# Performance work log

Hardware: AMD Instinct MI355X
Metric: run time of the kernel (lower is better)

Reference implementation:

```python
import jax, jax.numpy as jnp
import numpy as np

KV_LEN = 4096      # sliding-window length (init kv_len)
PAGE_SIZE = 16
SHIFT = 16         # hard-coded eviction shift in prefill_draft
BSZ = 4
SEQ_LEN = 512
HEADS = 16
HEAD_DIM = 128
PAGES = BSZ * KV_LEN // PAGE_SIZE  # 1024
ROPE_THETA = 10000.0


def _rope(x, positions):
    """Neox-style rotate-half RoPE. x: [B, L, H, D], positions: [L]."""
    d = x.shape[-1]
    inv_freq = 1.0 / (ROPE_THETA ** (jnp.arange(0, d, 2, dtype=jnp.float32) / d))  # [D/2]
    ang = positions.astype(jnp.float32)[:, None] * inv_freq[None, :]               # [L, D/2]
    cos = jnp.cos(ang)[None, :, None, :].astype(x.dtype)
    sin = jnp.sin(ang)[None, :, None, :].astype(x.dtype)
    x1, x2 = x[..., : d // 2], x[..., d // 2 :]
    return jnp.concatenate([x1 * cos - x2 * sin, x1 * sin + x2 * cos], axis=-1)


def setup_inputs() -> dict:
    key = jax.random.key(0)
    k1, k2, k3 = jax.random.split(key, 3)
    return {
        "k": jax.random.normal(k1, (BSZ * SEQ_LEN, HEADS, HEAD_DIM), jnp.float32),
        "v": jax.random.normal(k2, (BSZ * SEQ_LEN, HEADS, HEAD_DIM), jnp.float32),
        "draft_cache": jax.random.normal(k3, (PAGES, 2, PAGE_SIZE, HEADS, HEAD_DIM), jnp.float32),
        "kv_page_indices": jnp.arange(PAGES, dtype=jnp.int32),
        "bsz": BSZ,
        "context_len": KV_LEN,
        "seq_len": SEQ_LEN,
        "n_local_heads": HEADS,
        "head_dim": HEAD_DIM,
    }


def reference(k, v, draft_cache, kv_page_indices, bsz, context_len, seq_len, n_local_heads, head_dim):
    # Eviction branch of KVCache.prefill_draft (context_len + seq_len > kv_len):
    # gather paged cache -> sliding-window shift by SHIFT -> append new k/v -> re-RoPE keys -> scatter back to pages.
    pages_per_seq = kv_page_indices.shape[0] // bsz
    pages = kv_page_indices.reshape(bsz, pages_per_seq)                     # [B, P]
    # gather pages into per-sequence linear view: [B, 2, L, H, D]
    cache = draft_cache[pages]                                              # [B, P, 2, page, H, D]
    cache = jnp.transpose(cache, (0, 2, 1, 3, 4, 5)).reshape(
        bsz, 2, pages_per_seq * PAGE_SIZE, n_local_heads, head_dim)
    k_out, v_out = cache[:, 0], cache[:, 1]                                 # [B, L, H, D]

    k_val = k.reshape(bsz, seq_len, n_local_heads, head_dim)
    v_val = v.reshape(bsz, seq_len, n_local_heads, head_dim)

    keep = KV_LEN - SHIFT
    # shift window by SHIFT, append new tokens, keep last (kv_len - 16)
    new_k = jnp.concatenate([k_out[:, SHIFT:KV_LEN], k_val], axis=1)[:, -keep:]
    new_v = jnp.concatenate([v_out[:, SHIFT:KV_LEN], v_val], axis=1)[:, -keep:]

    k_full = k_out.at[:, :keep].set(new_k)
    v_full = v_out.at[:, :keep].set(new_v)

    # re-apply RoPE over the first kv_len key positions (offsets are zeros -> positions 0..kv_len-1)
    pos = jnp.arange(KV_LEN, dtype=jnp.int32)
    k_full = k_full.at[:, :KV_LEN].set(_rope(k_full[:, :KV_LEN], pos))

    # scatter back to paged layout: [max_num_pages, 2, page_size, H, D]
    kv = jnp.stack([k_full, v_full], axis=1)                                # [B, 2, L, H, D]
    kv = kv.reshape(bsz, 2, pages_per_seq, PAGE_SIZE, n_local_heads, head_dim)
    kv = jnp.transpose(kv, (0, 2, 1, 3, 4, 5)).reshape(-1, 2, PAGE_SIZE, n_local_heads, head_dim)
    rotated_kv = draft_cache.at[kv_page_indices].set(kv)
    return rotated_kv
```

## Files before the change

### kernel.cpp

```cpp
#include <hip/hip_runtime.h>
#include <math.h>

constexpr int KV_LEN    = 4096;
constexpr int PAGE_SZ   = 16;
constexpr int SHIFT     = 16;
constexpr int BSZ       = 4;
constexpr int SEQ_LEN   = 512;
constexpr int HEADS     = 16;
constexpr int HEAD_DIM  = 128;
constexpr int PAGES     = BSZ * KV_LEN / PAGE_SZ;
constexpr int PPS       = PAGES / BSZ;
constexpr int KEEP      = KV_LEN - SHIFT;
constexpr int CUT       = KEEP - SEQ_LEN;
constexpr int PAGE_STR  = 2 * PAGE_SZ * HEADS * HEAD_DIM;
constexpr int C_STR     = PAGE_SZ * HEADS * HEAD_DIM;
constexpr int S_STR     = HEADS * HEAD_DIM;

__global__ void build_inv(const int* __restrict__ idx, int* __restrict__ inv, int n) {
    int t = threadIdx.x;
    if (t < n) inv[t] = -1;
    __syncthreads();
    if (t < n) inv[idx[t]] = t;
}

__global__ __launch_bounds__(256) void kv_shift_rope(
    const float* __restrict__ kin, const float* __restrict__ vin,
    const float* __restrict__ dc,  const int*  __restrict__ pidx,
    const int*  __restrict__ inv,  float* __restrict__ out)
{
    int blk = blockIdx.x;
    int p   = blk >> 5;
    int rem = blk & 31;
    int c   = rem >> 4;
    int s   = rem & 15;

    int tid = threadIdx.x;
    int h   = tid >> 4;
    int d0  = (tid & 15) << 2;

    float* op   = out + (size_t)p * PAGE_STR + c * C_STR + s * S_STR;
    int    off1 = h * HEAD_DIM + d0;
    int    off2 = off1 + 64;

    int pos = inv[p];
    const float* sp;
    int j = 0;
    if (pos < 0) {
        sp = dc + (size_t)p * PAGE_STR + c * C_STR + s * S_STR;
    } else {
        int b  = pos >> 8;
        int pp = pos & (PPS - 1);
        j = pp * PAGE_SZ + s;
        if (j >= CUT && j < KEEP) {
            const float* base = (c == 0) ? kin : vin;
            sp = base + (size_t)(b * SEQ_LEN + (j - CUT)) * S_STR;
        } else {
            int t2 = (j < CUT) ? (j + SHIFT + SEQ_LEN) : j;
            int q  = t2 >> 4;
            int ss = t2 & 15;
            int srcpage = pidx[b * PPS + q];
            sp = dc + (size_t)srcpage * PAGE_STR + c * C_STR + ss * S_STR;
        }
    }

    float4 x1 = *(const float4*)(sp + off1);
    float4 x2 = *(const float4*)(sp + off2);

    if (pos >= 0 && c == 0) {
        const float neg_log2_theta_over_half = -0.20762050593046939f;
        float fj = (float)j;
        float o1[4], o2[4];
        float a1[4] = {x1.x, x1.y, x1.z, x1.w};
        float a2[4] = {x2.x, x2.y, x2.z, x2.w};
        #pragma unroll
        for (int i = 0; i < 4; i++) {
            float invf = exp2f((float)(d0 + i) * neg_log2_theta_over_half);
            float ang  = fj * invf;
            float sn, cs;
            sincosf(ang, &sn, &cs);
            o1[i] = a1[i] * cs - a2[i] * sn;
            o2[i] = a1[i] * sn + a2[i] * cs;
        }
        *(float4*)(op + off1) = make_float4(o1[0], o1[1], o1[2], o1[3]);
        *(float4*)(op + off2) = make_float4(o2[0], o2[1], o2[2], o2[3]);
    } else {
        *(float4*)(op + off1) = x1;
        *(float4*)(op + off2) = x2;
    }
}

extern "C" void kernel_launch(void* const* d_in, const int* in_sizes, int n_in,
                              void* d_out, int out_size, void* d_ws, size_t ws_size,
                              hipStream_t stream) {
    const float* kin  = (const float*)d_in[0];
    const float* vin  = (const float*)d_in[1];
    const float* dc   = (const float*)d_in[2];
    const int*   pidx = (const int*)d_in[3];
    int pages = in_sizes[3];

    int* inv = (int*)d_ws;
    build_inv<<<1, pages, 0, stream>>>(pidx, inv, pages);

    int grid = PAGES * 2 * PAGE_SZ;
    kv_shift_rope<<<grid, 256, 0, stream>>>(kin, vin, dc, pidx, inv, (float*)d_out);
}
```

Before: 457.0 us.

## Process whole pages per block with page-level source mapping and shuffle-based RoPE

Each block now copies or rotates an entire page half (16 slots) instead of one slot, resolving the source page once per block using page-aligned cut boundaries. RoPE partner halves are exchanged with warp shuffles instead of separate loads. This aims to amortize per-block index work and increase bytes per block, at the cost of fewer blocks and more sincos work per thread.

```diff
diff --git a/kernel.cpp b/kernel.cpp
--- a/kernel.cpp
+++ b/kernel.cpp
@@ -15,6 +15,9 @@
 constexpr int PAGE_STR  = 2 * PAGE_SZ * HEADS * HEAD_DIM;
 constexpr int C_STR     = PAGE_SZ * HEADS * HEAD_DIM;
 constexpr int S_STR     = HEADS * HEAD_DIM;
+constexpr int PP_CUT    = CUT / PAGE_SZ;
+constexpr int PP_KEEP   = KEEP / PAGE_SZ;
+constexpr int PP_SHIFT  = (SHIFT + SEQ_LEN) / PAGE_SZ;
 
 __global__ void build_inv(const int* __restrict__ idx, int* __restrict__ inv, int n) {
     int t = threadIdx.x;
@@ -29,63 +32,72 @@
     const int*  __restrict__ inv,  float* __restrict__ out)
 {
     int blk = blockIdx.x;
-    int p   = blk >> 5;
-    int rem = blk & 31;
-    int c   = rem >> 4;
-    int s   = rem & 15;
+    int p   = blk >> 1;
+    int c   = blk & 1;
+    int t   = threadIdx.x;
 
-    int tid = threadIdx.x;
-    int h   = tid >> 4;
-    int d0  = (tid & 15) << 2;
-
-    float* op   = out + (size_t)p * PAGE_STR + c * C_STR + s * S_STR;
-    int    off1 = h * HEAD_DIM + d0;
-    int    off2 = off1 + 64;
+    float* dst = out + (size_t)p * PAGE_STR + c * C_STR;
 
     int pos = inv[p];
-    const float* sp;
-    int j = 0;
+    const float* src;
+    int  j_base = 0;
+    bool rope   = false;
     if (pos < 0) {
-        sp = dc + (size_t)p * PAGE_STR + c * C_STR + s * S_STR;
+        src = dc + (size_t)p * PAGE_STR + c * C_STR;
     } else {
         int b  = pos >> 8;
         int pp = pos & (PPS - 1);
-        j = pp * PAGE_SZ + s;
-        if (j >= CUT && j < KEEP) {
-            const float* base = (c == 0) ? kin : vin;
-            sp = base + (size_t)(b * SEQ_LEN + (j - CUT)) * S_STR;
+        j_base = pp * PAGE_SZ;
+        rope   = (c == 0);
+        if (pp < PP_CUT) {
+            int sp_ = pidx[b * PPS + pp + PP_SHIFT];
+            src = dc + (size_t)sp_ * PAGE_STR + c * C_STR;
+        } else if (pp < PP_KEEP) {
+            const float* base = c ? vin : kin;
+            src = base + (size_t)(b * SEQ_LEN + j_base - CUT) * S_STR;
         } else {
-            int t2 = (j < CUT) ? (j + SHIFT + SEQ_LEN) : j;
-            int q  = t2 >> 4;
-            int ss = t2 & 15;
-            int srcpage = pidx[b * PPS + q];
-            sp = dc + (size_t)srcpage * PAGE_STR + c * C_STR + ss * S_STR;
+            int sp_ = pidx[b * PPS + pp];
+            src = dc + (size_t)sp_ * PAGE_STR + c * C_STR;
         }
     }
 
-    float4 x1 = *(const float4*)(sp + off1);
-    float4 x2 = *(const float4*)(sp + off2);
+    if (!rope) {
+        #pragma unroll 4
+        for (int it = 0; it < 32; ++it) {
+            int o = it * 1024 + t * 4;
+            *(float4*)(dst + o) = *(const float4*)(src + o);
+        }
+    } else {
+        const float NL = -0.20762050593046939f;
+        int   fi = (t * 4) & 63;
+        float f0 = exp2f((float)(fi + 0) * NL);
+        float f1 = exp2f((float)(fi + 1) * NL);
+        float f2 = exp2f((float)(fi + 2) * NL);
+        float f3 = exp2f((float)(fi + 3) * NL);
+        float sg = (((t * 4) & 64) == 0) ? -1.0f : 1.0f;
 
-    if (pos >= 0 && c == 0) {
-        const float neg_log2_theta_over_half = -0.20762050593046939f;
-        float fj = (float)j;
-        float o1[4], o2[4];
-        float a1[4] = {x1.x, x1.y, x1.z, x1.w};
-        float a2[4] = {x2.x, x2.y, x2.z, x2.w};
-        #pragma unroll
-        for (int i = 0; i < 4; i++) {
-            float invf = exp2f((float)(d0 + i) * neg_log2_theta_over_half);
-            float ang  = fj * invf;
-            float sn, cs;
-            sincosf(ang, &sn, &cs);
-            o1[i] = a1[i] * cs - a2[i] * sn;
-            o2[i] = a1[i] * sn + a2[i] * cs;
+        #pragma unroll 4
+        for (int it = 0; it < 32; ++it) {
+            int o = it * 1024 + t * 4;
+            float4 x = *(const float4*)(src + o);
+            float4 y;
+            y.x = __shfl_xor(x.x, 16);
+            y.y = __shfl_xor(x.y, 16);
+            y.z = __shfl_xor(x.z, 16);
+            y.w = __shfl_xor(x.w, 16);
+            float fj = (float)(j_base + (o >> 11));
+            float s0, c0, s1, c1, s2, c2, s3, c3;
+            sincosf(fj * f0, &s0, &c0);
+            sincosf(fj * f1, &s1, &c1);
+            sincosf(fj * f2, &s2, &c2);
+            sincosf(fj * f3, &s3, &c3);
+            float4 r;
+            r.x = fmaf(x.x, c0, sg * y.x * s0);
+            r.y = fmaf(x.y, c1, sg * y.y * s1);
+            r.z = fmaf(x.z, c2, sg * y.z * s2);
+            r.w = fmaf(x.w, c3, sg * y.w * s3);
+            *(float4*)(dst + o) = r;
         }
-        *(float4*)(op + off1) = make_float4(o1[0], o1[1], o1[2], o1[3]);
-        *(float4*)(op + off2) = make_float4(o2[0], o2[1], o2[2], o2[3]);
-    } else {
-        *(float4*)(op + off1) = x1;
-        *(float4*)(op + off2) = x2;
     }
 }
 
@@ -101,6 +113,5 @@
     int* inv = (int*)d_ws;
     build_inv<<<1, pages, 0, stream>>>(pidx, inv, pages);
 
-    int grid = PAGES * 2 * PAGE_SZ;
-    kv_shift_rope<<<grid, 256, 0, stream>>>(kin, vin, dc, pidx, inv, (float*)d_out);
+    kv_shift_rope<<<PAGES * 2, 256, 0, stream>>>(kin, vin, dc, pidx, inv, (float*)d_out);
 }
```

Result: slower. 474.2 us (+3.8%).
